# Performance work log

Measured on AMD Instinct MI355X. Metric: run time of the kernel, lower is better.

The kernel has to match this reference:

```python
import jax, jax.numpy as jnp
import numpy as np

EMBED = 2048
MLP = 8192
EPS = 1e-5


def setup_inputs() -> dict:
    key = jax.random.key(0)
    ks = jax.random.split(key, 16)
    s = 0.02
    inp = {
        "x": jax.random.normal(ks[0], (2, 2048, EMBED), dtype=jnp.float32),
        "wq": jax.random.normal(ks[1], (EMBED, EMBED), dtype=jnp.float32) * s,
        "bq": jnp.zeros((EMBED,), jnp.float32),
        "wk": jax.random.normal(ks[2], (EMBED, EMBED), dtype=jnp.float32) * s,
        "bk": jnp.zeros((EMBED,), jnp.float32),
        "wv": jax.random.normal(ks[3], (EMBED, EMBED), dtype=jnp.float32) * s,
        "bv": jnp.zeros((EMBED,), jnp.float32),
        "wd": jax.random.normal(ks[4], (EMBED, EMBED), dtype=jnp.float32) * s,
        "bd": jnp.zeros((EMBED,), jnp.float32),
        "ln_g": jnp.ones((EMBED,), jnp.float32),
        "ln_b": jnp.zeros((EMBED,), jnp.float32),
        "w1": jax.random.normal(ks[5], (MLP, EMBED), dtype=jnp.float32) * s,
        "b1": jnp.zeros((MLP,), jnp.float32),
        "w2": jax.random.normal(ks[6], (EMBED, MLP), dtype=jnp.float32) * s,
        "b2": jnp.zeros((EMBED,), jnp.float32),
    }
    return inp


def _layernorm(x, g, b):
    mu = jnp.mean(x, axis=-1, keepdims=True)
    var = jnp.mean(jnp.square(x - mu), axis=-1, keepdims=True)
    return (x - mu) * jax.lax.rsqrt(var + EPS) * g + b


def reference(x, wq, bq, wk, bk, wv, bv, wd, bd, ln_g, ln_b, w1, b1, w2, b2):
    # Single-head attention; scale uses full embed_dim (rotary_emb.dim == embed_dim).
    q = jnp.einsum("bse,fe->bsf", x, wq) + bq
    k = jnp.einsum("bse,fe->bsf", x, wk) + bk
    v = jnp.einsum("bse,fe->bsf", x, wv) + bv
    scores = jnp.einsum("bqe,bke->bqk", q, k) / jnp.sqrt(jnp.float32(EMBED))
    probs = jax.nn.softmax(scores, axis=-1)
    ctx = jnp.einsum("bqk,bke->bqe", probs, v)
    attn_out = jnp.einsum("bse,fe->bsf", ctx, wd) + bd
    # residual (dropout is identity in eval mode)
    h = x + attn_out
    h = _layernorm(h, ln_g, ln_b)
    mlp = jnp.einsum("bse,fe->bsf", h, w1) + b1
    mlp = jax.nn.gelu(mlp, approximate=False)
    mlp = jnp.einsum("bsf,ef->bse", mlp, w2) + b2
    return h + mlp
```

## Files before the change

### kernel.cpp

```cpp
#include <hip/hip_runtime.h>
#include <math.h>


#define SEQ 2048
#define EMB 2048
#define MLPD 8192

typedef __attribute__((ext_vector_type(8))) short short8;
typedef __attribute__((ext_vector_type(4))) float floatx4;
typedef unsigned short ushort;

__device__ __forceinline__ short f2bf(float f) {
  union { float f; unsigned u; } v; v.f = f;
  unsigned r = v.u + 0x7FFFu + ((v.u >> 16) & 1u);
  return (short)(r >> 16);
}
__device__ __forceinline__ float bf2f(ushort u) {
  union { unsigned u; float f; } v; v.u = ((unsigned)u) << 16;
  return v.f;
}

__device__ __forceinline__ void gload16(const ushort* g, ushort* l) {
  __builtin_amdgcn_global_load_lds(
      (__attribute__((address_space(1))) void*)g,
      (__attribute__((address_space(3))) void*)(unsigned)(unsigned long)l,
      16, 0, 0);
}

enum { EPI_QKV = 0, EPI_SCORES = 1, EPI_PV = 2, EPI_GELU = 4,
       EPI_VT = 5, EPI_SBF16 = 6 };

template<int EPI>
__global__ __launch_bounds__(512, 2)
void gemm256(const ushort* __restrict__ A, const ushort* __restrict__ B,
             const float* __restrict__ bias, void* __restrict__ Cp,
             int N, int K, int lda, int ldb, int ldc,
             long sA, long sB, long sC, float scale)
{
  extern __shared__ ushort lds[];
  const int t = threadIdx.x;
  const int lane = t & 63, w = t >> 6;
  const int wm = w >> 2, wn = w & 3;
  const long bm = (long)blockIdx.y * 256;
  const long bn = (long)blockIdx.x * 256;
  A += (long)blockIdx.z * sA;
  B += (long)blockIdx.z * sB;

  const int srow = (w << 3) + (lane >> 3);
  const int gcol = (lane & 7) ^ ((lane >> 3) & 7);
  const ushort* Ab = A + (bm + srow) * (long)lda + gcol * 8;
  const ushort* Bb = B + (bn + srow) * (long)ldb + gcol * 8;
  ushort* lw = lds + (w << 9);

#define STG_A0(LOFF, KK) do { gload16(Ab + (KK), lw + (LOFF)); \
    gload16(Ab + 64L * lda + (KK), lw + (LOFF) + 4096); } while (0)
#define STG_A1(LOFF, KK) do { gload16(Ab + 128L * lda + (KK), lw + (LOFF)); \
    gload16(Ab + 192L * lda + (KK), lw + (LOFF) + 4096); } while (0)
#define STG_B0(LOFF, KK) do { gload16(Bb + (KK), lw + (LOFF)); \
    gload16(Bb + 64L * ldb + (KK), lw + (LOFF) + 4096); } while (0)
#define STG_B1(LOFF, KK) do { gload16(Bb + 128L * ldb + (KK), lw + (LOFF)); \
    gload16(Bb + 192L * ldb + (KK), lw + (LOFF) + 4096); } while (0)

  const int l15 = lane & 15, q = lane >> 4, swz = l15 & 7;
  const int kx0 = (q ^ swz) << 3;
  const int kx1 = ((4 + q) ^ swz) << 3;
  const int arow = (wm << 13) + l15 * 64;
  const int brow = 16384 + ((wn >> 1) << 13) + ((wn & 1) << 12) + l15 * 64;

  floatx4 acc[8][4];
#pragma unroll
  for (int m = 0; m < 8; ++m)
#pragma unroll
    for (int n = 0; n < 4; ++n) acc[m][n] = (floatx4)0.0f;

  short8 A0[4], A1[4], B0[4], B1[4];

#define LDS8(IDX) (*(const short8*)&lds[IDX])
#define RD_ALK0(CB) do { _Pragma("unroll") for (int mf = 0; mf < 4; ++mf) \
    A0[mf] = LDS8((CB) + arow + mf * 1024 + kx0); } while (0)
#define RD_ALK1(CB) do { _Pragma("unroll") for (int mf = 0; mf < 4; ++mf) \
    A1[mf] = LDS8((CB) + arow + mf * 1024 + kx1); } while (0)
#define RD_AHK0(CB) do { _Pragma("unroll") for (int mf = 0; mf < 4; ++mf) \
    A0[mf] = LDS8((CB) + arow + (4 + mf) * 1024 + kx0); } while (0)
#define RD_AHK1(CB) do { _Pragma("unroll") for (int mf = 0; mf < 4; ++mf) \
    A1[mf] = LDS8((CB) + arow + (4 + mf) * 1024 + kx1); } while (0)
#define RD_BK0(CB) do { _Pragma("unroll") for (int nf = 0; nf < 4; ++nf) \
    B0[nf] = LDS8((CB) + brow + nf * 1024 + kx0); } while (0)
#define RD_BK1(CB) do { _Pragma("unroll") for (int nf = 0; nf < 4; ++nf) \
    B1[nf] = LDS8((CB) + brow + nf * 1024 + kx1); } while (0)

#define MMA16(MO, AX, BX) do {                                            \
    __builtin_amdgcn_s_setprio(1);                                        \
    _Pragma("unroll") for (int mf = 0; mf < 4; ++mf)                      \
      _Pragma("unroll") for (int nf = 0; nf < 4; ++nf)                    \
        acc[(MO)+mf][nf] = __builtin_amdgcn_mfma_f32_16x16x32_bf16(       \
            AX[mf], BX[nf], acc[(MO)+mf][nf], 0, 0, 0);                   \
    __builtin_amdgcn_s_setprio(0);                                        \
  } while (0)

#define BARR() __builtin_amdgcn_s_barrier()
#define VMC4  asm volatile("s_waitcnt vmcnt(4)" ::: "memory")

#define KTILE(CB, NB, K1, K2) do {                                        \
    RD_ALK0(CB); RD_BK0(CB); STG_A0((NB) + 0, K1);                        \
    MMA16(0, A0, B0); BARR();                                             \
    RD_ALK1(CB); RD_BK1(CB); STG_A1((NB) + 8192, K1);                     \
    MMA16(0, A1, B1); BARR();                                             \
    RD_AHK0(CB); STG_B0((CB) + 16384, K2);                                \
    MMA16(4, A0, B0); BARR();                                             \
    RD_AHK1(CB); STG_B1((CB) + 24576, K2);                                \
    MMA16(4, A1, B1); VMC4; BARR();                                       \
  } while (0)

  STG_A0(0, 0);              STG_A1(8192, 0);
  STG_B0(16384, 0);          STG_B1(24576, 0);
  {
    const int k1p = (K > 64) ? 64 : 0;
    STG_B0(32768 + 16384, k1p);
    STG_B1(32768 + 24576, k1p);
  }
  asm volatile("s_waitcnt vmcnt(4)" ::: "memory");
  BARR();

  const int NT = K >> 6;
  for (int kt = 0; kt < NT; kt += 2) {
    const int k1 = ((kt + 1 < NT) ? kt + 1 : NT - 1) << 6;
    const int k2 = ((kt + 2 < NT) ? kt + 2 : NT - 1) << 6;
    const int k3 = ((kt + 3 < NT) ? kt + 3 : NT - 1) << 6;
    KTILE(0,     32768, k1, k2);
    KTILE(32768, 0,     k2, k3);
  }
  asm volatile("s_waitcnt vmcnt(0)" ::: "memory");
#undef KTILE
#undef MMA16
#undef RD_ALK0
#undef RD_ALK1
#undef RD_AHK0
#undef RD_AHK1
#undef RD_BK0
#undef RD_BK1
#undef LDS8
#undef STG_A0
#undef STG_A1
#undef STG_B0
#undef STG_B1

  const int lq = lane >> 4;
#pragma unroll
  for (int mf = 0; mf < 8; ++mf) {
#pragma unroll
    for (int nf = 0; nf < 4; ++nf) {
#pragma unroll
      for (int i = 0; i < 4; ++i) {
        const long r = bm + wm * 128 + mf * 16 + lq * 4 + i;
        const long c = bn + wn * 64 + nf * 16 + l15;
        float val = acc[mf][nf][i];
        if constexpr (EPI == EPI_QKV) {
          val += bias[c];
          ((ushort*)Cp)[r * (long)ldc + c] = (ushort)f2bf(val);
        } else if constexpr (EPI == EPI_SCORES) {
          ((float*)Cp)[(long)blockIdx.z * sC + r * (long)ldc + c] = val * scale;
        } else {
          val += bias[c];
          float g = 0.5f * val * (1.0f + erff(val * 0.70710678118f));
          ((ushort*)Cp)[r * (long)ldc + c] = (ushort)f2bf(g);
        }
      }
    }
  }
}

template<int EPI>
__global__ __launch_bounds__(256)
void gemm_bt(const ushort* __restrict__ A, const ushort* __restrict__ B,
             const float* __restrict__ bias, void* __restrict__ Cp,
             int N, int K, int lda, int ldb, int ldc,
             long sA, long sB, long sC, float scale)
{
  __shared__ ushort As[128 * 64];
  __shared__ ushort Bs[128 * 64];

  const int t = threadIdx.x;
  const int lane = t & 63, wid = t >> 6;
  const int wm = wid >> 1, wn = wid & 1;
  const long bm = (long)blockIdx.y * 128;
  const long bn = (long)blockIdx.x * 128;
  A += (long)blockIdx.z * sA;
  B += (long)blockIdx.z * sB;

  const int srow = (wid << 3) + (lane >> 3);
  const int gcol = (lane & 7) ^ ((lane >> 3) & 7);
  const ushort* a0 = A + (bm + srow) * (long)lda + gcol * 8;
  const ushort* b0 = B + (bn + srow) * (long)ldb + gcol * 8;
  ushort* lA = As + (wid << 9);
  ushort* lB = Bs + (wid << 9);

  floatx4 acc[4][4];
#pragma unroll
  for (int m = 0; m < 4; ++m)
#pragma unroll
    for (int n = 0; n < 4; ++n) acc[m][n] = (floatx4)0.0f;

  const int l15 = lane & 15, q = lane >> 4, swz = l15 & 7;
  const int kx0 = (q ^ swz) << 3;
  const int kx1 = ((4 + q) ^ swz) << 3;
  const int abase = ((wm << 6) + l15) * 64;
  const int bbase = ((wn << 6) + l15) * 64;

  for (int kb = 0; kb < K; kb += 64) {
#pragma unroll
    for (int i = 0; i < 4; ++i) {
      gload16(a0 + (32L * i) * lda + kb, lA + i * 2048);
      gload16(b0 + (32L * i) * ldb + kb, lB + i * 2048);
    }
    __syncthreads();

    short8 a0r[4], a1r[4], b0r[4], b1r[4];
#pragma unroll
    for (int m = 0; m < 4; ++m) {
      a0r[m] = *reinterpret_cast<const short8*>(&As[abase + m * 1024 + kx0]);
      a1r[m] = *reinterpret_cast<const short8*>(&As[abase + m * 1024 + kx1]);
    }
#pragma unroll
    for (int n = 0; n < 4; ++n) {
      b0r[n] = *reinterpret_cast<const short8*>(&Bs[bbase + n * 1024 + kx0]);
      b1r[n] = *reinterpret_cast<const short8*>(&Bs[bbase + n * 1024 + kx1]);
    }
    __builtin_amdgcn_s_setprio(1);
#pragma unroll
    for (int m = 0; m < 4; ++m)
#pragma unroll
      for (int n = 0; n < 4; ++n) {
        acc[m][n] = __builtin_amdgcn_mfma_f32_16x16x32_bf16(a0r[m], b0r[n], acc[m][n], 0, 0, 0);
        acc[m][n] = __builtin_amdgcn_mfma_f32_16x16x32_bf16(a1r[m], b1r[n], acc[m][n], 0, 0, 0);
      }
    __builtin_amdgcn_s_setprio(0);
    __syncthreads();
  }

  const int lq = lane >> 4;
#pragma unroll
  for (int m = 0; m < 4; ++m) {
#pragma unroll
    for (int n = 0; n < 4; ++n) {
#pragma unroll
      for (int i = 0; i < 4; ++i) {
        const long r = bm + wm * 64 + m * 16 + lq * 4 + i;
        const long c = bn + wn * 64 + n * 16 + l15;
        float val = acc[m][n][i];
        if constexpr (EPI == EPI_SBF16) {
          ((ushort*)Cp)[(long)blockIdx.z * sC + r * (long)ldc + c] =
              (ushort)f2bf(val * scale);
        } else if constexpr (EPI == EPI_PV) {
          ((ushort*)Cp)[(long)blockIdx.z * sC + r * (long)ldc + c] = (ushort)f2bf(val);
        } else if constexpr (EPI == EPI_VT) {
          val += bias[r];
          ((ushort*)Cp)[(long)blockIdx.z * sC + r * (long)ldc + c] = (ushort)f2bf(val);
        }
      }
    }
  }
}

struct CvtSeg { const float* src; ushort* dst; long end; };

__global__ __launch_bounds__(256)
void cvt_all(const float* x,  ushort* xb,
             const float* wq, const float* wk, ushort* wqkb,
             const float* wv, ushort* wvb,
             const float* wd, ushort* wdb,
             const float* w1, ushort* w1b,
             const float* w2, ushort* w2b,
             const float* bq, const float* bk, float* bqk)
{
  if (blockIdx.x < 16) {
    const int i = blockIdx.x * 256 + threadIdx.x;
    bqk[i] = (i < 2048) ? bq[i] : bk[i - 2048];
  }
  const long gi = ((long)blockIdx.x * 256 + threadIdx.x) * 8;
  const float* src;
  ushort* dst;
  long off;
  if (gi < 8388608L)        { src = x;  dst = xb;             off = 0; }
  else if (gi < 12582912L)  { src = wq; dst = wqkb;           off = 8388608L; }
  else if (gi < 16777216L)  { src = wk; dst = wqkb + 4194304; off = 12582912L; }
  else if (gi < 20971520L)  { src = wv; dst = wvb;            off = 16777216L; }
  else if (gi < 25165824L)  { src = wd; dst = wdb;            off = 20971520L; }
  else if (gi < 41943040L)  { src = w1; dst = w1b;            off = 25165824L; }
  else                      { src = w2; dst = w2b;            off = 41943040L; }
  const long i = gi - off;
  float4 a = *reinterpret_cast<const float4*>(src + i);
  float4 b = *reinterpret_cast<const float4*>(src + i + 4);
  short8 v;
  v[0] = f2bf(a.x); v[1] = f2bf(a.y); v[2] = f2bf(a.z); v[3] = f2bf(a.w);
  v[4] = f2bf(b.x); v[5] = f2bf(b.y); v[6] = f2bf(b.z); v[7] = f2bf(b.w);
  *reinterpret_cast<short8*>(dst + i) = v;
}

__global__ __launch_bounds__(256)
void reduce2(const float* __restrict__ p0, const float* __restrict__ p1,
             const float* __restrict__ bias, const float* __restrict__ res,
             float* __restrict__ out)
{
  const long i = ((long)blockIdx.x * 256 + threadIdx.x) * 8;
  const int c = (int)(i & 2047);
  float4 a0 = *(const float4*)(p0 + i),  a1 = *(const float4*)(p0 + i + 4);
  float4 q0 = *(const float4*)(p1 + i),  q1 = *(const float4*)(p1 + i + 4);
  float4 r0 = *(const float4*)(res + i), r1 = *(const float4*)(res + i + 4);
  float4 b0 = *(const float4*)(bias + c), b1 = *(const float4*)(bias + c + 4);
  float4 o0 = {a0.x + q0.x + r0.x + b0.x, a0.y + q0.y + r0.y + b0.y,
               a0.z + q0.z + r0.z + b0.z, a0.w + q0.w + r0.w + b0.w};
  float4 o1 = {a1.x + q1.x + r1.x + b1.x, a1.y + q1.y + r1.y + b1.y,
               a1.z + q1.z + r1.z + b1.z, a1.w + q1.w + r1.w + b1.w};
  *(float4*)(out + i) = o0;
  *(float4*)(out + i + 4) = o1;
}

__global__ __launch_bounds__(256)
void softmax_rows(const ushort* __restrict__ S, ushort* __restrict__ P) {
  const long row = blockIdx.x;
  const ushort* src = S + row * 2048;
  const int t = threadIdx.x, lane = t & 63, wid = t >> 6;
  short8 raw = *reinterpret_cast<const short8*>(src + t * 8);
  float v[8];
#pragma unroll
  for (int i = 0; i < 8; ++i) v[i] = bf2f((ushort)raw[i]);
  float m = v[0];
#pragma unroll
  for (int i = 1; i < 8; ++i) m = fmaxf(m, v[i]);
#pragma unroll
  for (int o = 32; o; o >>= 1) m = fmaxf(m, __shfl_xor(m, o));
  __shared__ float rm[4], rs[4];
  if (!lane) rm[wid] = m;
  __syncthreads();
  m = fmaxf(fmaxf(rm[0], rm[1]), fmaxf(rm[2], rm[3]));
  float e[8], s = 0.f;
#pragma unroll
  for (int i = 0; i < 8; ++i) { e[i] = __expf(v[i] - m); s += e[i]; }
#pragma unroll
  for (int o = 32; o; o >>= 1) s += __shfl_xor(s, o);
  if (!lane) rs[wid] = s;
  __syncthreads();
  s = rs[0] + rs[1] + rs[2] + rs[3];
  const float inv = 1.0f / s;
  short8 wv;
#pragma unroll
  for (int i = 0; i < 8; ++i) wv[i] = f2bf(e[i] * inv);
  *reinterpret_cast<short8*>(P + row * 2048 + t * 8) = wv;
}

__global__ __launch_bounds__(256)
void layernorm_fused(const float* __restrict__ p0, const float* __restrict__ p1,
                     const float* __restrict__ bias, const float* __restrict__ res,
                     const float* __restrict__ g, const float* __restrict__ bb,
                     float* __restrict__ H, ushort* __restrict__ Hb) {
  const long row = blockIdx.x;
  const long base = row * 2048;
  const int t = threadIdx.x, lane = t & 63, wid = t >> 6;
  const long i = base + t * 8;
  const int c0 = t * 8;
  float v[8];
  {
    float4 a0 = *(const float4*)(p0 + i),  a1 = *(const float4*)(p0 + i + 4);
    float4 q0 = *(const float4*)(p1 + i),  q1 = *(const float4*)(p1 + i + 4);
    float4 r0 = *(const float4*)(res + i), r1 = *(const float4*)(res + i + 4);
    float4 b0 = *(const float4*)(bias + c0), b1 = *(const float4*)(bias + c0 + 4);
    v[0] = a0.x + q0.x + r0.x + b0.x; v[1] = a0.y + q0.y + r0.y + b0.y;
    v[2] = a0.z + q0.z + r0.z + b0.z; v[3] = a0.w + q0.w + r0.w + b0.w;
    v[4] = a1.x + q1.x + r1.x + b1.x; v[5] = a1.y + q1.y + r1.y + b1.y;
    v[6] = a1.z + q1.z + r1.z + b1.z; v[7] = a1.w + q1.w + r1.w + b1.w;
  }
  float s = 0.f, ss = 0.f;
#pragma unroll
  for (int i2 = 0; i2 < 8; ++i2) { s += v[i2]; ss += v[i2] * v[i2]; }
#pragma unroll
  for (int o = 32; o; o >>= 1) { s += __shfl_xor(s, o); ss += __shfl_xor(ss, o); }
  __shared__ float r1s[4], r2s[4];
  if (!lane) { r1s[wid] = s; r2s[wid] = ss; }
  __syncthreads();
  s = r1s[0] + r1s[1] + r1s[2] + r1s[3];
  ss = r2s[0] + r2s[1] + r2s[2] + r2s[3];
  const float mu = s * (1.0f / 2048.0f);
  const float var = ss * (1.0f / 2048.0f) - mu * mu;
  const float inv = rsqrtf(var + 1e-5f);
  float o0[8];
  short8 wv;
#pragma unroll
  for (int i2 = 0; i2 < 8; ++i2) {
    const int c = c0 + i2;
    o0[i2] = (v[i2] - mu) * inv * g[c] + bb[c];
    wv[i2] = f2bf(o0[i2]);
  }
  float4 w0 = {o0[0], o0[1], o0[2], o0[3]}, w1 = {o0[4], o0[5], o0[6], o0[7]};
  *reinterpret_cast<float4*>(H + i) = w0;
  *reinterpret_cast<float4*>(H + i + 4) = w1;
  *reinterpret_cast<short8*>(Hb + i) = wv;
}

extern "C" void kernel_launch(void* const* d_in, const int* in_sizes, int n_in,
                              void* d_out, int out_size, void* d_ws, size_t ws_size,
                              hipStream_t stream) {
  const float* x    = (const float*)d_in[0];
  const float* wq   = (const float*)d_in[1];
  const float* bq   = (const float*)d_in[2];
  const float* wk   = (const float*)d_in[3];
  const float* bk   = (const float*)d_in[4];
  const float* wv   = (const float*)d_in[5];
  const float* bv   = (const float*)d_in[6];
  const float* wd   = (const float*)d_in[7];
  const float* bd   = (const float*)d_in[8];
  const float* ln_g = (const float*)d_in[9];
  const float* ln_b = (const float*)d_in[10];
  const float* w1   = (const float*)d_in[11];
  const float* b1   = (const float*)d_in[12];
  const float* w2   = (const float*)d_in[13];
  const float* b2   = (const float*)d_in[14];
  float* out = (float*)d_out;

  (void)hipFuncSetAttribute((const void*)&gemm256<EPI_QKV>,
      hipFuncAttributeMaxDynamicSharedMemorySize, 131072);
  (void)hipFuncSetAttribute((const void*)&gemm256<EPI_GELU>,
      hipFuncAttributeMaxDynamicSharedMemorySize, 131072);
  (void)hipFuncSetAttribute((const void*)&gemm256<EPI_SCORES>,
      hipFuncAttributeMaxDynamicSharedMemorySize, 131072);

  char* p = (char*)d_ws;
  const size_t MB = 1048576;
  ushort* wdb    = (ushort*)(p + 0 * MB);
  ushort* w1b    = (ushort*)(p + 8 * MB);
  ushort* w2b    = (ushort*)(p + 40 * MB);
  float*  bqk    = (float*) (p + 72 * MB);
  ushort* xb     = (ushort*)(p + 73 * MB);
  ushort* probs  = xb;
  ushort* qk     = (ushort*)(p + 89 * MB);
  ushort* wqkb   = (ushort*)(p + 121 * MB);
  ushort* vT     = (ushort*)(p + 121 * MB);
  ushort* wvb    = (ushort*)(p + 137 * MB);
  ushort* scoresb= (ushort*)(p + 137 * MB);
  float*  partA  = (float*) (p + 89 * MB);
  ushort* mlpb   = (ushort*)(p + 89 * MB);
  float*  h      = (float*) (p + 153 * MB);
  ushort* hb     = (ushort*)(p + 185 * MB);
  ushort* ctx    = (ushort*)(p + 201 * MB);
  float*  partM0 = (float*) (p + 0 * MB);
  float*  partM1 = (float*) (p + 201 * MB);

  const dim3 blk(256), blk512(512);
  const long SQ = (long)SEQ * SEQ;

  cvt_all<<<28672, blk, 0, stream>>>(
      x, xb, wq, wk, wqkb, wv, wvb, wd, wdb, w1, w1b, w2, w2b, bq, bk, bqk);

  gemm256<EPI_QKV><<<dim3(16, 16, 1), blk512, 131072, stream>>>(
      xb, wqkb, bqk, qk, 4096, 2048, 2048, 2048, 4096, 0, 0, 0, 1.f);

  gemm_bt<EPI_VT><<<dim3(16, 16, 2), blk, 0, stream>>>(
      wvb, xb, bv, vT, 2048, 2048, 2048, 2048, 2048,
      0, SQ, SQ, 1.f);

  gemm_bt<EPI_SBF16><<<dim3(16, 16, 2), blk, 0, stream>>>(
      qk, qk + 2048, nullptr, scoresb, 2048, 2048, 4096, 4096, 2048,
      2048L * 4096, 2048L * 4096, SQ, 0.022097086912079608f);

  softmax_rows<<<dim3(4096), blk, 0, stream>>>(scoresb, probs);

  gemm_bt<EPI_PV><<<dim3(16, 16, 2), blk, 0, stream>>>(
      probs, vT, nullptr, ctx, 2048, 2048, 2048, 2048, 2048,
      SQ, SQ, SQ, 1.f);

  gemm256<EPI_SCORES><<<dim3(8, 16, 2), blk512, 131072, stream>>>(
      ctx, wdb, nullptr, partA, 2048, 1024, 2048, 2048, 2048,
      1024, 1024, 8388608, 1.f);

  layernorm_fused<<<4096, blk, 0, stream>>>(
      partA, partA + 8388608, bd, x, ln_g, ln_b, h, hb);

  gemm256<EPI_GELU><<<dim3(32, 16, 1), blk512, 131072, stream>>>(
      hb, w1b, b1, mlpb, 8192, 2048, 2048, 2048, 8192, 0, 0, 0, 1.f);

  gemm256<EPI_SCORES><<<dim3(8, 16, 2), blk512, 131072, stream>>>(
      mlpb, w2b, nullptr, partM0, 2048, 4096, 8192, 8192, 2048,
      4096, 4096, (long)(201 * MB / 4), 1.f);
  reduce2<<<4096, blk, 0, stream>>>(partM0, partM1, b2, h, out);
}
```

Baseline: 609.8 us.

## Double-buffer LDS tiles in gemm_bt to overlap global loads with MFMA

Replaces the single-buffered A/B shared tiles in gemm_bt with a 64KB double buffer. The loads for the next K tile are issued before the current tile's MFMAs, and one barrier per tile replaces the two. This hides global-to-LDS load latency behind compute, at the cost of doubled LDS use, which may lower occupancy. An odd tile count or the clamped final prefetch could cause redundant loads.

```diff
diff --git a/kernel.cpp b/kernel.cpp
--- a/kernel.cpp
+++ b/kernel.cpp
@@ -177,8 +177,7 @@
              int N, int K, int lda, int ldb, int ldc,
              long sA, long sB, long sC, float scale)
 {
-  __shared__ ushort As[128 * 64];
-  __shared__ ushort Bs[128 * 64];
+  __shared__ ushort lds[32768];
 
   const int t = threadIdx.x;
   const int lane = t & 63, wid = t >> 6;
@@ -192,8 +191,11 @@
   const int gcol = (lane & 7) ^ ((lane >> 3) & 7);
   const ushort* a0 = A + (bm + srow) * (long)lda + gcol * 8;
   const ushort* b0 = B + (bn + srow) * (long)ldb + gcol * 8;
-  ushort* lA = As + (wid << 9);
-  ushort* lB = Bs + (wid << 9);
+  const int lw = (wid << 9);
+
+#define STG(CB, KK) do { _Pragma("unroll") for (int i = 0; i < 4; ++i) {   \
+    gload16(a0 + (32L * i) * lda + (KK), lds + (CB) + lw + i * 2048);      \
+    gload16(b0 + (32L * i) * ldb + (KK), lds + (CB) + 8192 + lw + i * 2048); } } while (0)
 
   floatx4 acc[4][4];
 #pragma unroll
@@ -205,38 +207,45 @@
   const int kx0 = (q ^ swz) << 3;
   const int kx1 = ((4 + q) ^ swz) << 3;
   const int abase = ((wm << 6) + l15) * 64;
-  const int bbase = ((wn << 6) + l15) * 64;
-
-  for (int kb = 0; kb < K; kb += 64) {
-#pragma unroll
-    for (int i = 0; i < 4; ++i) {
-      gload16(a0 + (32L * i) * lda + kb, lA + i * 2048);
-      gload16(b0 + (32L * i) * ldb + kb, lB + i * 2048);
-    }
-    __syncthreads();
-
-    short8 a0r[4], a1r[4], b0r[4], b1r[4];
-#pragma unroll
-    for (int m = 0; m < 4; ++m) {
-      a0r[m] = *reinterpret_cast<const short8*>(&As[abase + m * 1024 + kx0]);
-      a1r[m] = *reinterpret_cast<const short8*>(&As[abase + m * 1024 + kx1]);
-    }
-#pragma unroll
-    for (int n = 0; n < 4; ++n) {
-      b0r[n] = *reinterpret_cast<const short8*>(&Bs[bbase + n * 1024 + kx0]);
-      b1r[n] = *reinterpret_cast<const short8*>(&Bs[bbase + n * 1024 + kx1]);
-    }
-    __builtin_amdgcn_s_setprio(1);
-#pragma unroll
-    for (int m = 0; m < 4; ++m)
-#pragma unroll
-      for (int n = 0; n < 4; ++n) {
-        acc[m][n] = __builtin_amdgcn_mfma_f32_16x16x32_bf16(a0r[m], b0r[n], acc[m][n], 0, 0, 0);
-        acc[m][n] = __builtin_amdgcn_mfma_f32_16x16x32_bf16(a1r[m], b1r[n], acc[m][n], 0, 0, 0);
-      }
-    __builtin_amdgcn_s_setprio(0);
-    __syncthreads();
-  }
+  const int bbase = 8192 + ((wn << 6) + l15) * 64;
+
+#define TILE(CB, NB, KK) do {                                              \
+    STG(NB, KK);        \
+    short8 a0r[4], a1r[4], b0r[4], b1r[4];                                 \
+    _Pragma("unroll") for (int m = 0; m < 4; ++m) {                        \
+      a0r[m] = *(const short8*)&lds[(CB) + abase + m * 1024 + kx0];        \
+      a1r[m] = *(const short8*)&lds[(CB) + abase + m * 1024 + kx1];        \
+    }                                                                      \
+    _Pragma("unroll") for (int n = 0; n < 4; ++n) {                        \
+      b0r[n] = *(const short8*)&lds[(CB) + bbase + n * 1024 + kx0];        \
+      b1r[n] = *(const short8*)&lds[(CB) + bbase + n * 1024 + kx1];        \
+    }                                                                      \
+    __builtin_amdgcn_s_setprio(1);                                         \
+    _Pragma("unroll") for (int m = 0; m < 4; ++m)                          \
+      _Pragma("unroll") for (int n = 0; n < 4; ++n) {                      \
+        acc[m][n] = __builtin_amdgcn_mfma_f32_16x16x32_bf16(               \
+            a0r[m], b0r[n], acc[m][n], 0, 0, 0);                           \
+        acc[m][n] = __builtin_amdgcn_mfma_f32_16x16x32_bf16(               \
+            a1r[m], b1r[n], acc[m][n], 0, 0, 0);                           \
+      }                                                                    \
+    __builtin_amdgcn_s_setprio(0);                                         \
+    asm volatile("s_waitcnt vmcnt(0)" ::: "memory");                       \
+    __builtin_amdgcn_s_barrier();                                          \
+  } while (0)
+
+  STG(0, 0);
+  asm volatile("s_waitcnt vmcnt(0)" ::: "memory");
+  __builtin_amdgcn_s_barrier();
+
+  const int NT = K >> 6;
+  for (int kt = 0; kt < NT; kt += 2) {
+    const int k1 = ((kt + 1 < NT) ? kt + 1 : NT - 1) << 6;
+    const int k2 = ((kt + 2 < NT) ? kt + 2 : NT - 1) << 6;
+    TILE(0,     16384, k1);
+    TILE(16384, 0,     k2);
+  }
+#undef TILE
+#undef STG
 
   const int lq = lane >> 4;
 #pragma unroll
@@ -261,8 +270,6 @@
     }
   }
 }
-
-struct CvtSeg { const float* src; ushort* dst; long end; };
 
 __global__ __launch_bounds__(256)
 void cvt_all(const float* x,  ushort* xb,
```

Result: faster. 582.1 us (-4.5%).
